# Optimization experiments

Hardware: AMD Instinct MI355X
Metric: run time of the kernel (lower is better)

Reference implementation:

```python
import jax, jax.numpy as jnp
import numpy as np

N, C, H, W = 64, 256, 28, 28
INTER = 128  # in_channels // reduction
STD = 0.01   # init std of the 1x1 convs


def setup_inputs() -> dict:
    key = jax.random.key(0)
    k_x, k_idx, k_wq, k_wv, k_lam = jax.random.split(key, 5)
    x = jax.random.normal(k_x, (N, C, H, W), dtype=jnp.float32)
    lam = jax.random.uniform(k_lam, (), dtype=jnp.float32)
    index = jax.random.randint(k_idx, (N,), 0, N)
    # query 1x1 conv (shared for q and k since x_qk_concat=False -> key is None)
    Wq = jax.random.normal(k_wq, (INTER, C), dtype=jnp.float32) * STD
    bq = jnp.zeros((INTER,), dtype=jnp.float32)
    # value 1x1 conv -> 1 channel
    Wv = jax.random.normal(k_wv, (1, C), dtype=jnp.float32) * STD
    bv = jnp.zeros((1,), dtype=jnp.float32)
    return {"x": x, "lam": lam, "index": index, "Wq": Wq, "bq": bq,
            "Wv": Wv, "bv": bv, "scale_factor": 8}


def _conv1x1(x, w, b):
    # x: [n,c,h,w], w: [o,c], b: [o] -> [n,o,h,w]
    return jnp.einsum('nchw,oc->nohw', x, w) + b[None, :, None, None]


def reference(x, lam, index, Wq, bq, Wv, bv, scale_factor):
    n, c, h, w = x.shape
    hw = h * w
    x_lam = x               # [n,c,h,w]
    x_lam_ = x[index]       # shuffled pair
    # value: 1x1 conv to 1 channel -> [n, hw, 1]
    v = _conv1x1(x_lam_, Wv, bv).reshape(n, 1, hw).transpose(0, 2, 1)
    # query / key share the same conv (key is None when x_qk_concat=False)
    q = _conv1x1(x_lam, Wq, bq).reshape(n, INTER, hw).transpose(0, 2, 1)  # [n,hw,inter]
    k = _conv1x1(x_lam_, Wq, bq).reshape(n, INTER, hw)                    # [n,inter,hw]
    # embedded gaussian similarity, forced fp32, scaled by sqrt(inter)
    scores = jnp.einsum('nqc,nck->nqk', q.astype(jnp.float32), k.astype(jnp.float32))
    scores = scores / jnp.float32(np.sqrt(INTER))
    pw = jax.nn.softmax(scores, axis=-1)  # [n,hw,hw]
    mask = jnp.einsum('nqk,nko->nqo', pw, v.astype(jnp.float32)).reshape(n, 1, h, w)
    # bilinear upsample (align_corners=False semantics) then sigmoid
    mask = jax.image.resize(mask, (n, 1, h * scale_factor, w * scale_factor),
                            method='bilinear')
    mask = jax.nn.sigmoid(mask)
    # results['mask'] = cat([1 - m, m], dim=1)
    return jnp.concatenate([1.0 - mask, mask], axis=1)
```

## Files before the change

kernel.cpp:

```cpp
#include <hip/hip_runtime.h>
#include <math.h>

#define NB    64
#define CIN   256
#define HH    28
#define WW    28
#define HW    784
#define INTER 128

typedef __bf16 bf16x8 __attribute__((ext_vector_type(8)));
typedef float  f32x4  __attribute__((ext_vector_type(4)));

#define SCALE 0.35709723f

#define GLB(p) ((const __attribute__((address_space(1))) void*)(p))
#define LDSP(p) ((__attribute__((address_space(3))) void*)(p))

__device__ __forceinline__ unsigned int bfbits(float f) {
    unsigned int u = __builtin_bit_cast(unsigned int, f);
    return (u + 0x7fffu + ((u >> 16) & 1u)) >> 16;
}

__global__ __launch_bounds__(256) void initw_kernel(
    const float* __restrict__ Wq, unsigned short* __restrict__ Wbh)
{
    const int e  = blockIdx.x * 256 + threadIdx.x;
    const int j  = e & 7;
    const int l  = (e >> 3) & 63;
    const int it = (e >> 9) & 7;
    const int s  = e >> 12;
    const int i  = it * 16 + (l & 15);
    const int c  = s * 32 + ((l >> 4) & 3) * 8 + j;
    Wbh[e] = (unsigned short)bfbits(Wq[i * CIN + c] * SCALE);
}

__global__ __launch_bounds__(256, 5) void proj_kernel(
    const float* __restrict__ x,
    const unsigned short* __restrict__ Wfh,
    const float* __restrict__ bq,
    const float* __restrict__ Wv, const float* __restrict__ bv,
    unsigned short* __restrict__ Yb, float* __restrict__ vAll)
{
    __shared__ float          Xs [2][32 * 64];
    __shared__ unsigned short Whs[2][4096];

    const int ptile = blockIdx.x;
    const int n     = blockIdx.y;
    const int t     = threadIdx.x;
    const int l     = t & 63;
    const int w     = t >> 6;
    const int pl    = l & 15;
    const int g     = l >> 4;
    const int p0    = ptile * 64;

    const float* xn = x + (size_t)n * (CIN * HW);

    const int kk    = pl ^ (w << 2);
    const int psrc  = min(p0 + kk * 4, HW - 4);

    const int slot  = ((w * 16 + pl) >> 2) ^ (g << 2);
    const int rbyte = slot * 4 + (pl & 3);

    f32x4 acc[8];
#pragma unroll
    for (int it = 0; it < 8; ++it) acc[it] = (f32x4){0.f, 0.f, 0.f, 0.f};
    float vpart = 0.0f;

#pragma unroll
    for (int q = 0; q < 2; ++q) {
        const int rt = w * 8 + q * 4 + g;
        __builtin_amdgcn_global_load_lds(GLB(xn + (size_t)rt * HW + psrc),
                                         LDSP(&Xs[0][(w * 8 + q * 4) * 64]), 16, 0, 0);
        const int chunk = (w * 2 + q) * 512;
        __builtin_amdgcn_global_load_lds(GLB(Wfh + chunk + l * 8),
                                         LDSP(&Whs[0][chunk]), 16, 0, 0);
    }
    __syncthreads();

    int cur = 0;
    for (int s = 0; s < 8; ++s) {
        if (s < 7) {
#pragma unroll
            for (int q = 0; q < 2; ++q) {
                const int rt = w * 8 + q * 4 + g;
                __builtin_amdgcn_global_load_lds(
                    GLB(xn + (size_t)((s + 1) * 32 + rt) * HW + psrc),
                    LDSP(&Xs[cur ^ 1][(w * 8 + q * 4) * 64]), 16, 0, 0);
                const int chunk = (w * 2 + q) * 512;
                __builtin_amdgcn_global_load_lds(
                    GLB(Wfh + (s + 1) * 4096 + chunk + l * 8),
                    LDSP(&Whs[cur ^ 1][chunk]), 16, 0, 0);
            }
        }

        float xv[8];
#pragma unroll
        for (int j = 0; j < 8; ++j)
            xv[j] = Xs[cur][(g * 8 + j) * 64 + rbyte];

        const float4 wv0 = *(const float4*)(Wv + s * 32 + g * 8);
        const float4 wv1 = *(const float4*)(Wv + s * 32 + g * 8 + 4);
        vpart = fmaf(xv[0], wv0.x, fmaf(xv[1], wv0.y,
                fmaf(xv[2], wv0.z, fmaf(xv[3], wv0.w, vpart))));
        vpart = fmaf(xv[4], wv1.x, fmaf(xv[5], wv1.y,
                fmaf(xv[6], wv1.z, fmaf(xv[7], wv1.w, vpart))));

        bf16x8 ah;
#pragma unroll
        for (int j = 0; j < 8; ++j) ah[j] = (__bf16)xv[j];

#pragma unroll
        for (int it = 0; it < 8; ++it) {
            const bf16x8 wh = *(const bf16x8*)&Whs[cur][it * 512 + l * 8];
            acc[it] = __builtin_amdgcn_mfma_f32_16x16x32_bf16(ah, wh, acc[it], 0, 0, 0);
        }

        __syncthreads();
        cur ^= 1;
    }

    const int p0w = p0 + w * 16;

    vpart += __shfl_xor(vpart, 16);
    vpart += __shfl_xor(vpart, 32);
    if (g == 0 && p0w + pl < HW)
        vAll[n * HW + p0w + pl] = vpart + bv[0];

#pragma unroll
    for (int it = 0; it < 8; ++it) {
        const int i = it * 16 + pl;
        const float bb = bq[i] * SCALE;
#pragma unroll
        for (int r = 0; r < 4; ++r) {
            const int pr = p0w + g * 4 + r;
            if (pr < HW)
                Yb[((size_t)n * HW + pr) * INTER + i] =
                    (unsigned short)bfbits(acc[it][r] + bb);
        }
    }
}

__global__ __launch_bounds__(256) void attn_kernel(
    const unsigned short* __restrict__ Yb, const float* __restrict__ vAll,
    const int* __restrict__ index, float* __restrict__ maskbuf)
{
    __shared__ float red[2][4][112];

    const int n   = blockIdx.x;
    const int qt  = blockIdx.y;
    const int q0  = qt * 112;
    const int t   = threadIdx.x;
    const int l   = t & 63;
    const int w   = t >> 6;
    const int idx = index[n];

    const unsigned short* Qg = Yb + (size_t)n   * (HW * INTER);
    const unsigned short* Kg = Yb + (size_t)idx * (HW * INTER);
    const float*          Vg = vAll + (size_t)idx * HW;

    const int ql = l & 15;
    const int g  = l >> 4;

    bf16x8 qf[7][4];
#pragma unroll
    for (int qg = 0; qg < 7; ++qg) {
        const int qrow = q0 + qg * 16 + ql;
#pragma unroll
        for (int ic = 0; ic < 4; ++ic)
            qf[qg][ic] = *(const bf16x8*)(Qg + (size_t)qrow * INTER + ic * 32 + g * 8);
    }

    float ll[7] = {0.f, 0.f, 0.f, 0.f, 0.f, 0.f, 0.f};
    float oo[7] = {0.f, 0.f, 0.f, 0.f, 0.f, 0.f, 0.f};

    const int NT = (w == 0) ? 13 : 12;
    const unsigned short* Ka = Kg + (size_t)(w * 16 + ql) * INTER + g * 8;
    const float*          Va = Vg + w * 16 + g * 4;

    bf16x8 afA[4], afB[4];
    float4 vvA, vvB;

#define LOADK(kt, dst, vdst)                                               \
    {                                                                      \
        const unsigned short* kp = Ka + (size_t)(kt) * (64 * INTER);       \
        dst[0] = *(const bf16x8*)(kp);                                     \
        dst[1] = *(const bf16x8*)(kp + 32);                                \
        dst[2] = *(const bf16x8*)(kp + 64);                                \
        dst[3] = *(const bf16x8*)(kp + 96);                                \
        vdst = *(const float4*)(Va + (kt) * 64);                           \
    }

#define PROCESS(af, vv)                                                    \
    {                                                                      \
        _Pragma("unroll")                                                  \
        for (int qg = 0; qg < 7; ++qg) {                                   \
            f32x4 acc = (f32x4){0.f, 0.f, 0.f, 0.f};                       \
            _Pragma("unroll")                                              \
            for (int ic = 0; ic < 4; ++ic)                                 \
                acc = __builtin_amdgcn_mfma_f32_16x16x32_bf16(             \
                    af[ic], qf[qg][ic], acc, 0, 0, 0);                     \
            const float e0 = exp2f(acc[0]);                                \
            const float e1 = exp2f(acc[1]);                                \
            const float e2 = exp2f(acc[2]);                                \
            const float e3 = exp2f(acc[3]);                                \
            ll[qg] += (e0 + e1) + (e2 + e3);                               \
            oo[qg] = fmaf(e0, vv.x, fmaf(e1, vv.y,                         \
                     fmaf(e2, vv.z, fmaf(e3, vv.w, oo[qg]))));             \
        }                                                                  \
    }

    LOADK(0, afA, vvA);
    int kt = 0;
    for (; kt + 1 < NT; kt += 2) {
        LOADK(kt + 1, afB, vvB);
        PROCESS(afA, vvA);
        if (kt + 2 < NT) LOADK(kt + 2, afA, vvA);
        PROCESS(afB, vvB);
    }
    if (kt < NT) PROCESS(afA, vvA);

#undef LOADK
#undef PROCESS

#pragma unroll
    for (int qg = 0; qg < 7; ++qg) {
        ll[qg] += __shfl_xor(ll[qg], 16); ll[qg] += __shfl_xor(ll[qg], 32);
        oo[qg] += __shfl_xor(oo[qg], 16); oo[qg] += __shfl_xor(oo[qg], 32);
    }
    if (g == 0) {
#pragma unroll
        for (int qg = 0; qg < 7; ++qg) {
            red[0][w][qg * 16 + ql] = ll[qg];
            red[1][w][qg * 16 + ql] = oo[qg];
        }
    }
    __syncthreads();
    if (t < 112) {
        const float L = red[0][0][t] + red[0][1][t] + red[0][2][t] + red[0][3][t];
        const float O = red[1][0][t] + red[1][1][t] + red[1][2][t] + red[1][3][t];
        maskbuf[n * HW + q0 + t] = O / L;
    }
}

__global__ __launch_bounds__(256) void upsample_kernel(
    const float* __restrict__ maskbuf, float* __restrict__ out)
{
    const int gid = blockIdx.x * 256 + threadIdx.x;
    const int n  = gid / (224 * 56);
    const int r  = gid - n * (224 * 56);
    const int oy = r / 56;
    const int xq = r - oy * 56;

    const float iy = (oy + 0.5f) * 0.125f - 0.5f;
    const int   y0 = (int)floorf(iy);
    const float fy = iy - (float)y0;
    const int y0c = max(y0, 0), y1c = min(y0 + 1, HH - 1);
    const float* mrow = maskbuf + n * HW;

    float res[4];
#pragma unroll
    for (int j = 0; j < 4; ++j) {
        const int   ox = (xq << 2) + j;
        const float ix = (ox + 0.5f) * 0.125f - 0.5f;
        const int   x0 = (int)floorf(ix);
        const float fx = ix - (float)x0;
        const int x0c = max(x0, 0), x1c = min(x0 + 1, WW - 1);
        const float v00 = mrow[y0c * WW + x0c], v01 = mrow[y0c * WW + x1c];
        const float v10 = mrow[y1c * WW + x0c], v11 = mrow[y1c * WW + x1c];
        const float m = (v00 * (1.0f - fx) + v01 * fx) * (1.0f - fy)
                      + (v10 * (1.0f - fx) + v11 * fx) * fy;
        res[j] = 1.0f / (1.0f + __expf(-m));
    }

    float4 pos = make_float4(res[0], res[1], res[2], res[3]);
    float4 neg = make_float4(1.0f - res[0], 1.0f - res[1],
                             1.0f - res[2], 1.0f - res[3]);
    const size_t base = (size_t)n * 2 * 50176 + (size_t)oy * 224 + (xq << 2);
    *(float4*)(out + base)         = neg;
    *(float4*)(out + base + 50176) = pos;
}

extern "C" void kernel_launch(void* const* d_in, const int* in_sizes, int n_in,
                              void* d_out, int out_size, void* d_ws, size_t ws_size,
                              hipStream_t stream) {
    const float* x     = (const float*)d_in[0];
    const int*   index = (const int*)d_in[2];
    const float* Wq    = (const float*)d_in[3];
    const float* bq    = (const float*)d_in[4];
    const float* Wv    = (const float*)d_in[5];
    const float* bv    = (const float*)d_in[6];

    float* out = (float*)d_out;
    unsigned short* Yb  = (unsigned short*)d_out;
    unsigned short* Wbh = Yb + (size_t)NB * HW * INTER;
    float* vAll  = (float*)d_ws;
    float* maskb = vAll + NB * HW;

    initw_kernel<<<128, 256, 0, stream>>>(Wq, Wbh);
    proj_kernel<<<dim3(13, NB), 256, 0, stream>>>(x, Wbh, bq, Wv, bv, Yb, vAll);
    attn_kernel<<<dim3(NB, 7), 256, 0, stream>>>(Yb, vAll, index, maskb);
    upsample_kernel<<<3136, 256, 0, stream>>>(maskb, out);
}
```

Before: 62.19 us.

## Stream K/V tiles into LDS via async global_load_lds triple buffering

The attention kernel now stages K tiles and V values into a per-wave, triple-buffered LDS ring using direct global-to-LDS loads, instead of prefetching them into registers two tiles at a time. Loads run up to three tiles ahead, gated by explicit vmcnt waits, and the K rows use an XOR swizzle to avoid LDS bank conflicts on readback. The intent is to hide global memory latency and free the VGPRs that held prefetched fragments. In exchange the block uses about 55 KB of LDS, which can limit blocks per CU, and the hand-written waitcnt counts must match the number of loads issued per tile.

```diff
diff --git a/kernel.cpp b/kernel.cpp
--- a/kernel.cpp
+++ b/kernel.cpp
@@ -144,7 +144,8 @@
     const unsigned short* __restrict__ Yb, const float* __restrict__ vAll,
     const int* __restrict__ index, float* __restrict__ maskbuf)
 {
-    __shared__ float red[2][4][112];
+    __shared__ __align__(16) unsigned char ldsraw[52224 + 3584];
+    float* red = (float*)(ldsraw + 52224);
 
     const int n   = blockIdx.x;
     const int qt  = blockIdx.y;
@@ -160,6 +161,7 @@
 
     const int ql = l & 15;
     const int g  = l >> 4;
+    const int wbase = w * 13056;
 
     bf16x8 qf[7][4];
 #pragma unroll
@@ -174,53 +176,65 @@
     float oo[7] = {0.f, 0.f, 0.f, 0.f, 0.f, 0.f, 0.f};
 
     const int NT = (w == 0) ? 13 : 12;
-    const unsigned short* Ka = Kg + (size_t)(w * 16 + ql) * INTER + g * 8;
-    const float*          Va = Vg + w * 16 + g * 4;
-
-    bf16x8 afA[4], afB[4];
-    float4 vvA, vvB;
-
-#define LOADK(kt, dst, vdst)                                               \
-    {                                                                      \
-        const unsigned short* kp = Ka + (size_t)(kt) * (64 * INTER);       \
-        dst[0] = *(const bf16x8*)(kp);                                     \
-        dst[1] = *(const bf16x8*)(kp + 32);                                \
-        dst[2] = *(const bf16x8*)(kp + 64);                                \
-        dst[3] = *(const bf16x8*)(kp + 96);                                \
-        vdst = *(const float4*)(Va + (kt) * 64);                           \
-    }
-
-#define PROCESS(af, vv)                                                    \
-    {                                                                      \
-        _Pragma("unroll")                                                  \
-        for (int qg = 0; qg < 7; ++qg) {                                   \
-            f32x4 acc = (f32x4){0.f, 0.f, 0.f, 0.f};                       \
-            _Pragma("unroll")                                              \
-            for (int ic = 0; ic < 4; ++ic)                                 \
-                acc = __builtin_amdgcn_mfma_f32_16x16x32_bf16(             \
-                    af[ic], qf[qg][ic], acc, 0, 0, 0);                     \
-            const float e0 = exp2f(acc[0]);                                \
-            const float e1 = exp2f(acc[1]);                                \
-            const float e2 = exp2f(acc[2]);                                \
-            const float e3 = exp2f(acc[3]);                                \
-            ll[qg] += (e0 + e1) + (e2 + e3);                               \
-            oo[qg] = fmaf(e0, vv.x, fmaf(e1, vv.y,                         \
-                     fmaf(e2, vv.z, fmaf(e3, vv.w, oo[qg]))));             \
-        }                                                                  \
-    }
-
-    LOADK(0, afA, vvA);
-    int kt = 0;
-    for (; kt + 1 < NT; kt += 2) {
-        LOADK(kt + 1, afB, vvB);
-        PROCESS(afA, vvA);
-        if (kt + 2 < NT) LOADK(kt + 2, afA, vvA);
-        PROCESS(afB, vvB);
-    }
-    if (kt < NT) PROCESS(afA, vvA);
-
-#undef LOADK
-#undef PROCESS
+
+#define ISSUE(kt_, slot_)                                                   \
+    {                                                                       \
+        const int sb = wbase + (slot_) * 4352;                              \
+        _Pragma("unroll")                                                   \
+        for (int j = 0; j < 4; ++j) {                                       \
+            const int row = (j << 2) + (l >> 4);                            \
+            const int c   = (l & 15) ^ row;                                 \
+            const unsigned short* src =                                     \
+                Kg + (size_t)((kt_) * 64 + w * 16 + row) * INTER + c * 8;   \
+            __builtin_amdgcn_global_load_lds(GLB(src),                      \
+                LDSP(ldsraw + sb + j * 1024 + l * 16), 16, 0, 0);           \
+        }                                                                   \
+        __builtin_amdgcn_global_load_lds(                                   \
+            GLB(Vg + (kt_) * 64 + w * 16 + (l & 15)),                       \
+            LDSP(ldsraw + sb + 4096 + l * 4), 4, 0, 0);                     \
+    }
+
+    ISSUE(0, 0)
+    ISSUE(1, 1)
+    ISSUE(2, 2)
+
+    int slot = 0;
+    for (int kt = 0; kt < NT; ++kt) {
+        if (kt + 2 < NT)      asm volatile("s_waitcnt vmcnt(10)" ::: "memory");
+        else if (kt + 1 < NT) asm volatile("s_waitcnt vmcnt(5)"  ::: "memory");
+        else                  asm volatile("s_waitcnt vmcnt(0)"  ::: "memory");
+        __builtin_amdgcn_sched_barrier(0);
+
+        const int sb = wbase + slot * 4352;
+        bf16x8 af[4];
+#pragma unroll
+        for (int ic = 0; ic < 4; ++ic) {
+            const int s_ = (ic * 4 + g) ^ ql;
+            af[ic] = *(const bf16x8*)(ldsraw + sb + ql * 256 + s_ * 16);
+        }
+        const float4 vv = *(const float4*)(ldsraw + sb + 4096 + g * 16);
+
+#pragma unroll
+        for (int qg = 0; qg < 7; ++qg) {
+            f32x4 acc = (f32x4){0.f, 0.f, 0.f, 0.f};
+#pragma unroll
+            for (int ic = 0; ic < 4; ++ic)
+                acc = __builtin_amdgcn_mfma_f32_16x16x32_bf16(
+                    af[ic], qf[qg][ic], acc, 0, 0, 0);
+            const float e0 = exp2f(acc[0]);
+            const float e1 = exp2f(acc[1]);
+            const float e2 = exp2f(acc[2]);
+            const float e3 = exp2f(acc[3]);
+            ll[qg] += (e0 + e1) + (e2 + e3);
+            oo[qg] = fmaf(e0, vv.x, fmaf(e1, vv.y,
+                     fmaf(e2, vv.z, fmaf(e3, vv.w, oo[qg]))));
+        }
+
+        if (kt + 3 < NT) ISSUE(kt + 3, slot)
+
+        slot = (slot == 2) ? 0 : slot + 1;
+    }
+#undef ISSUE
 
 #pragma unroll
     for (int qg = 0; qg < 7; ++qg) {
@@ -230,14 +244,16 @@
     if (g == 0) {
 #pragma unroll
         for (int qg = 0; qg < 7; ++qg) {
-            red[0][w][qg * 16 + ql] = ll[qg];
-            red[1][w][qg * 16 + ql] = oo[qg];
+            red[(0 * 4 + w) * 112 + qg * 16 + ql] = ll[qg];
+            red[(1 * 4 + w) * 112 + qg * 16 + ql] = oo[qg];
         }
     }
     __syncthreads();
     if (t < 112) {
-        const float L = red[0][0][t] + red[0][1][t] + red[0][2][t] + red[0][3][t];
-        const float O = red[1][0][t] + red[1][1][t] + red[1][2][t] + red[1][3][t];
+        const float L = red[0 * 448 + 0 * 112 + t] + red[0 * 448 + 1 * 112 + t]
+                      + red[0 * 448 + 2 * 112 + t] + red[0 * 448 + 3 * 112 + t];
+        const float O = red[1 * 448 + 0 * 112 + t] + red[1 * 448 + 1 * 112 + t]
+                      + red[1 * 448 + 2 * 112 + t] + red[1 * 448 + 3 * 112 + t];
         maskbuf[n * HW + q0 + t] = O / L;
     }
 }
```

Result: no change. 62.62 us (+0.7%).
